# Optimization experiments

Measured on AMD Instinct MI355X. Metric: run time of the kernel, lower is better.

## Reference

```python
import jax, jax.numpy as jnp
import numpy as np
from jax import lax

T, B, D_IN, D_DAY, H, D_OUT = 64, 32, 4096, 256, 256, 942


def setup_inputs() -> dict:
    key = jax.random.key(0)
    ks = jax.random.split(key, 18)
    s = 0.05
    def rn(k, shape):
        return jax.random.normal(k, shape, jnp.float32) * s
    return {
        "x": jax.random.uniform(ks[0], (T, B, D_IN), jnp.float32),
        "W_emb": rn(ks[1], (D_DAY, D_IN)), "b_emb": rn(ks[2], (D_DAY,)),
        "Wih_f": rn(ks[3], (3 * H, D_DAY)), "Whh_f": rn(ks[4], (3 * H, H)),
        "bih_f": rn(ks[5], (3 * H,)), "bhh_f": rn(ks[6], (3 * H,)),
        "Wih_r": rn(ks[7], (3 * H, D_DAY)), "Whh_r": rn(ks[8], (3 * H, H)),
        "bih_r": rn(ks[9], (3 * H,)), "bhh_r": rn(ks[10], (3 * H,)),
        "attn_w": rn(ks[11], (2 * H,)), "attn_b": rn(ks[12], ()),
        "W_ao": rn(ks[13], (D_DAY, 4 * H)), "b_ao": rn(ks[14], (D_DAY,)),
        "W_o": rn(ks[15], (D_OUT, D_DAY)), "b_o": rn(ks[16], (D_OUT,)),
    }


def _gru_cell(xt, h, Wih, Whh, bih, bhh):
    # PyTorch nn.GRU cell math
    gi = xt @ Wih.T + bih          # [B, 3H]
    gh = h @ Whh.T + bhh           # [B, 3H]
    ir, iz, inn = jnp.split(gi, 3, axis=-1)
    hr, hz, hn = jnp.split(gh, 3, axis=-1)
    r = jax.nn.sigmoid(ir + hr)
    z = jax.nn.sigmoid(iz + hz)
    n = jnp.tanh(inn + r * hn)
    return (1.0 - z) * n + z * h


def _run_gru(seq, Wih, Whh, bih, bhh):
    # seq: [L, B, D] -> all hidden states [L, B, H], h0 = zeros
    h0 = jnp.zeros((seq.shape[1], H), seq.dtype)
    def step(h, xt):
        h2 = _gru_cell(xt, h, Wih, Whh, bih, bhh)
        return h2, h2
    return lax.scan(step, h0, seq)[1]


def reference(x, W_emb, b_emb, Wih_f, Whh_f, bih_f, bhh_f,
              Wih_r, Whh_r, bih_r, bhh_r, attn_w, attn_b,
              W_ao, b_ao, W_o, b_o):
    day_emb = jnp.einsum('tbi,di->tbd', x, W_emb) + b_emb       # [T,B,Dday]

    # Forward GRU over the prefix [:i+1] equals the first i+1 states of one full run.
    fwd = _run_gru(day_emb, Wih_f, Whh_f, bih_f, bhh_f)          # [T,B,H]

    # Reverse GRU is recomputed per timestep on the flipped prefix (O(T^2)).
    i_idx = jnp.arange(T)
    j_idx = jnp.arange(T)
    gather = jnp.clip(i_idx[:, None] - j_idx[None, :], 0)        # [T,T]
    rev_in = day_emb[gather]                                     # [T,T,B,Dday]; row i, step j = day_emb[i-j]
    rev = jax.vmap(lambda s: _run_gru(s, Wih_r, Whh_r, bih_r, bhh_r))(rev_in)  # [T,T,B,H]

    # Attention scores on concat(fwd, rev) without materializing the 2H concat:
    w_f, w_r = attn_w[:H], attn_w[H:]
    scores = (jnp.einsum('tbh,h->tb', fwd, w_f)[None, :, :]
              + jnp.einsum('itbh,h->itb', rev, w_r) + attn_b)    # [T(i),T(t),B]
    valid = j_idx[None, :] <= i_idx[:, None]                     # t <= i
    scores = jnp.where(valid[:, :, None], scores, -jnp.inf)
    alpha = jax.nn.softmax(scores, axis=1)                       # softmax over prefix time

    counts = (i_idx + 1).astype(day_emb.dtype)[:, None, None]    # mean over i+1 steps
    c_fwd = jnp.einsum('itb,tbh->ibh', alpha, fwd) / counts      # [T,B,H]
    c_rev = jnp.einsum('itb,itbh->ibh', alpha, rev) / counts     # [T,B,H]
    rev_last = rev[i_idx, i_idx]                                 # rnn_h[-1] reverse half, [T,B,H]

    h_t = jnp.concatenate([c_fwd, c_rev, fwd, rev_last], axis=-1)  # [T,B,4H]
    h_t_out = h_t @ W_ao.T + b_ao                                # [T,B,Dday]
    return jax.nn.sigmoid(h_t_out @ W_o.T + b_o)                 # [T,B,D_OUT]
```

## Files before the change

### kernel.cpp

```cpp
#include <hip/hip_runtime.h>
#include <hip/hip_bf16.h>


typedef __bf16 bf16x8 __attribute__((ext_vector_type(8)));
typedef __bf16 bf16x4 __attribute__((ext_vector_type(4)));
typedef float  f32x4  __attribute__((ext_vector_type(4)));
typedef int    int4v  __attribute__((ext_vector_type(4)));

static constexpr float NEG_L2E = -1.442695041f;
static constexpr float TWO_L2E =  2.885390082f;

static constexpr size_t OFF_PK_EMB = 0;
static constexpr size_t OFF_PK_IH  = 2097152;
static constexpr size_t OFF_WQ     = 2883584;
static constexpr size_t OFF_WSC    = 3276800;
static constexpr size_t OFF_PK_AO  = 3670016;
static constexpr size_t OFF_PK_O   = 4194304;
static constexpr size_t OFF_DAY    = 4685824;
static constexpr size_t OFF_GIT    = 5734400;
static constexpr size_t OFF_BC     = 12025856;
static constexpr size_t OFF_REV    = 18317312;
static constexpr size_t OFF_FWD    = 52396032;
static constexpr size_t OFF_HT     = 53444608;
static constexpr size_t OFF_TMP1   = 57638912;
static constexpr size_t OFF_XB     = OFF_REV;

__device__ __forceinline__ float sigf(float x) {
    return __builtin_amdgcn_rcpf(1.f + __expf(-x));
}

#define LDS_BARRIER() asm volatile("s_waitcnt lgkmcnt(0)\n\ts_barrier" ::: "memory")

__global__ __launch_bounds__(256) void pack_misc(
    const float* __restrict__ We,  const float* __restrict__ Wir, const float* __restrict__ Wif,
    const float* __restrict__ Wao, const float* __restrict__ Wo,  const float* __restrict__ x,
    const float* __restrict__ Whr, const float* __restrict__ Whf,
    const float* __restrict__ bih_r, const float* __restrict__ bih_f,
    const float* __restrict__ bhh_r, const float* __restrict__ bhh_f,
    __bf16* pe, __bf16* pi, __bf16* pao, __bf16* po, __bf16* xb,
    signed char* __restrict__ wq, float* __restrict__ wscale, float* __restrict__ bc)
{
    int b = blockIdx.x;
    if (b >= 5048) {
        int rowb = (b - 5048) * 4 + (threadIdx.x >> 6);
        int t = threadIdx.x & 63;
        int dir = (rowb >= 768) ? 1 : 0;
        int n = rowb - dir * 768;
        const float* src = (dir ? Whf : Whr) + (size_t)n * 256;
        float4 wv = ((const float4*)src)[t];
        float m = fmaxf(fmaxf(fabsf(wv.x), fabsf(wv.y)), fmaxf(fabsf(wv.z), fabsf(wv.w)));
#pragma unroll
        for (int off = 32; off > 0; off >>= 1) m = fmaxf(m, __shfl_xor(m, off));
        m = fmaxf(m, 1e-20f);
        float inv = 127.f / m;
        int q0 = (int)__builtin_rintf(wv.x * inv);
        int q1 = (int)__builtin_rintf(wv.y * inv);
        int q2 = (int)__builtin_rintf(wv.z * inv);
        int q3 = (int)__builtin_rintf(wv.w * inv);
        int pk = (q0 & 0xff) | ((q1 & 0xff) << 8) | ((q2 & 0xff) << 16) | ((q3 & 0xff) << 24);
        int dlane = (n & 15) | (((t >> 2) & 3) << 4);
        size_t byte = (size_t)dir * 196608 + ((size_t)(n >> 4) * 4 + (t >> 4)) * 1024
                    + (size_t)dlane * 16 + (t & 3) * 4;
        *(int*)(wq + byte) = pk;
        if (t == 0) {
            float gc = (n < 512) ? NEG_L2E : TWO_L2E;
            wscale[rowb] = m * (1.f / 16129.f) * gc;
            const float* bi = dir ? bih_f : bih_r;
            const float* bh = dir ? bhh_f : bhh_r;
            bc[rowb] = (n < 512) ? (bi[n] + bh[n]) * NEG_L2E : bi[n] * TWO_L2E;
        }
        return;
    }
    if (b >= 952) {
        size_t base = ((size_t)(b - 952) * 256 + threadIdx.x) * 8;
        float4 v0 = *(const float4*)(x + base);
        float4 v1 = *(const float4*)(x + base + 4);
        bf16x8 o;
        o[0]=(__bf16)v0.x; o[1]=(__bf16)v0.y; o[2]=(__bf16)v0.z; o[3]=(__bf16)v0.w;
        o[4]=(__bf16)v1.x; o[5]=(__bf16)v1.y; o[6]=(__bf16)v1.z; o[7]=(__bf16)v1.w;
        *(bf16x8*)(xb + base) = o;
        return;
    }
    const float* src; __bf16* dst; int Nsrc, k32l, b0; bool ih = false;
    if (b < 512)      { src = We;  dst = pe;          Nsrc = 256; k32l = 7; b0 = 0;   }
    else if (b < 608) { src = Wir; dst = pi;          Nsrc = 768; k32l = 3; b0 = 512; ih = true; }
    else if (b < 704) { src = Wif; dst = pi + 196608; Nsrc = 768; k32l = 3; b0 = 608; ih = true; }
    else if (b < 832) { src = Wao; dst = pao;         Nsrc = 256; k32l = 5; b0 = 704; }
    else              { src = Wo;  dst = po;          Nsrc = 942; k32l = 3; b0 = 832; }
    int t8   = (b - b0) * 256 + threadIdx.x;
    int lane = t8 & 63;
    int K32  = 1 << k32l;
    int K    = K32 << 5;
    int ks   = (t8 >> 6) & (K32 - 1);
    int nt   = t8 >> (6 + k32l);
    int n    = nt * 16 + (lane & 15);
    int k0   = ks * 32 + ((lane >> 4) << 3);
    bf16x8 o;
    if (n < Nsrc) {
        const float* sp = src + (size_t)n * K + k0;
        float4 v0 = *(const float4*)sp;
        float4 v1 = *(const float4*)(sp + 4);
        float s = ih ? ((n < 512) ? NEG_L2E : TWO_L2E) : 1.f;
        o[0]=(__bf16)(v0.x*s); o[1]=(__bf16)(v0.y*s); o[2]=(__bf16)(v0.z*s); o[3]=(__bf16)(v0.w*s);
        o[4]=(__bf16)(v1.x*s); o[5]=(__bf16)(v1.y*s); o[6]=(__bf16)(v1.z*s); o[7]=(__bf16)(v1.w*s);
    } else {
#pragma unroll
        for (int q = 0; q < 8; q++) o[q] = (__bf16)0.f;
    }
    *(bf16x8*)(dst + (size_t)t8 * 8) = o;
}

template<int MODE, int KDIM, int NTILES, int CSTRIDE, int NREAL>
__global__ __launch_bounds__(256) void gemm_k(
    const __bf16* __restrict__ Ap, const __bf16* __restrict__ Bp, void* __restrict__ Cp,
    const float* __restrict__ bias)
{
    __shared__ __align__(16) __bf16 As[32][88];
    const int tid = threadIdx.x;
    const int w = tid >> 6, lane = tid & 63, c = lane & 15, quad = lane >> 4;
    const int mb = blockIdx.x, nb = blockIdx.y;
    constexpr int K32 = KDIM / 32;
    constexpr int NK  = KDIM / 64;
    constexpr int NT_W = NTILES / 2;
    const int wrow = w & 1, ncol0 = (w >> 1) * NT_W;

    f32x4 acc[NT_W];
#pragma unroll
    for (int nt = 0; nt < NT_W; nt++) acc[nt] = (f32x4){0.f, 0.f, 0.f, 0.f};

    const int row = tid >> 3, kp = (tid & 7) * 8;
    uint4 pb;
    auto issue  = [&](int kb) { pb = *(const uint4*)(Ap + (size_t)(mb * 32 + row) * KDIM + kb * 64 + kp); };
    auto commit = [&]() { *(uint4*)&As[row][kp] = pb; };

    bf16x8 bcur[2][NT_W], bnxt[2][NT_W];
    auto loadB = [&](int kb, bf16x8 (&dst)[2][NT_W]) {
#pragma unroll
        for (int kk = 0; kk < 2; kk++)
#pragma unroll
            for (int nt = 0; nt < NT_W; nt++)
                dst[kk][nt] = *(const bf16x8*)(Bp +
                    ((size_t)((nb * NTILES + ncol0 + nt) * K32 + kb * 2 + kk) * 64 + lane) * 8);
    };

    issue(0);
    loadB(0, bcur);
    for (int kb = 0; kb < NK; kb++) {
        commit();
        __syncthreads();
        if (kb + 1 < NK) { issue(kb + 1); loadB(kb + 1, bnxt); }
#pragma unroll
        for (int kk = 0; kk < 2; kk++) {
            bf16x8 a = *(const bf16x8*)&As[wrow * 16 + c][kk * 32 + quad * 8];
#pragma unroll
            for (int nt = 0; nt < NT_W; nt++)
                acc[nt] = __builtin_amdgcn_mfma_f32_16x16x32_bf16(a, bcur[kk][nt], acc[nt], 0, 0, 0);
        }
        if (kb + 1 < NK) {
#pragma unroll
            for (int kk = 0; kk < 2; kk++)
#pragma unroll
                for (int nt = 0; nt < NT_W; nt++) bcur[kk][nt] = bnxt[kk][nt];
        }
        __syncthreads();
    }

#pragma unroll
    for (int nt = 0; nt < NT_W; nt++) {
        int n = nb * (NTILES * 16) + (ncol0 + nt) * 16 + c;
        float bv = (n < NREAL) ? bias[n] : 0.f;
#pragma unroll
        for (int r0 = 0; r0 < 4; r0++) {
            int m = mb * 32 + wrow * 16 + quad * 4 + r0;
            float v = acc[nt][r0] + bv;
            if constexpr (MODE == 0) ((__bf16*)Cp)[(size_t)m * CSTRIDE + n] = (__bf16)v;
            else { if (n < NREAL) ((float*)Cp)[(size_t)m * CSTRIDE + n] = sigf(v); }
        }
    }
}

__global__ __launch_bounds__(1024, 4) void gru_recurrent(
    const signed char* __restrict__ wq, const float* __restrict__ wscale,
    const float* __restrict__ bhh_r, const float* __restrict__ bhh_f,
    const __bf16* __restrict__ Gi,
    __bf16* __restrict__ revb, __bf16* __restrict__ fwdb)
{
    __shared__ __align__(16) signed char hbuf[2][16][272];
    const int tid = threadIdx.x;
    const int w = tid >> 6, lane = tid & 63, c = lane & 15, quad = lane >> 4;
    const int bid = blockIdx.x;
    const bool isF = (bid < 2);
    const int ia = isF ? 63 : (63 - ((bid - 2) >> 1));
    const int b0 = (bid & 1) << 4;
    const int steps = ia + 1;
    const float* bhh = isF ? bhh_f : bhh_r;
    __bf16* outb = isF ? fwdb : (revb + ((size_t)(ia * (ia + 1) / 2)) * 8192);
    const int dirb = isF ? 768 : 0;

    const int4v* pw = (const int4v*)(wq + (isF ? 196608 : 0));
    int4v bw[3][4];
#pragma unroll
    for (int g = 0; g < 3; g++)
#pragma unroll
        for (int ks = 0; ks < 4; ks++)
            bw[g][ks] = pw[(size_t)((g * 16 + w) * 4 + ks) * 64 + lane];

    const int dq = (w << 4) + (quad << 2);
    f32x4 sc[3];
#pragma unroll
    for (int g = 0; g < 3; g++) sc[g] = *(const f32x4*)&wscale[dirb + g * 256 + dq];
    f32x4 bnv = *(const f32x4*)&bhh[512 + dq];
#pragma unroll
    for (int q = 0; q < 4; q++) bnv[q] *= TWO_L2E;

    float hreg[4] = {0.f, 0.f, 0.f, 0.f};
    for (int idx = tid; idx < 2 * 16 * 272 / 4; idx += 1024) ((int*)hbuf)[idx] = 0;
    __syncthreads();

    const __bf16* grow = Gi + (size_t)((isF ? 0 : ia) * 32 + b0 + c) * 1536 + dirb + dq;
    const long gstep = isF ? (32 * 1536) : -(32 * 1536);
    __bf16* go = outb + (size_t)(b0 + c) * 256 + dq;

    bf16x4 gcur[3], gnxt[3];
#pragma unroll
    for (int g = 0; g < 3; g++) gcur[g] = *(const bf16x4*)(grow + g * 256);

    for (int j = 0; j < steps; j++) {
        const int rb = j & 1, wbuf = rb ^ 1;
        const bool more = (j + 1 < steps);

        if (more) {
            grow += gstep;
#pragma unroll
            for (int g = 0; g < 3; g++) gnxt[g] = *(const bf16x4*)(grow + g * 256);
        }

        int4v a0 = {0,0,0,0}, a1 = {0,0,0,0}, a2 = {0,0,0,0};
#pragma unroll
        for (int ks = 0; ks < 4; ks++) {
            int4v av = *(const int4v*)&hbuf[rb][c][ks * 64 + (quad << 4)];
            a0 = __builtin_amdgcn_mfma_i32_16x16x64_i8(bw[0][ks], av, a0, 0, 0, 0);
            a1 = __builtin_amdgcn_mfma_i32_16x16x64_i8(bw[1][ks], av, a1, 0, 0, 0);
            a2 = __builtin_amdgcn_mfma_i32_16x16x64_i8(bw[2][ks], av, a2, 0, 0, 0);
        }

        int pk = 0;
        bf16x4 hb;
#pragma unroll
        for (int r0 = 0; r0 < 4; r0++) {
            float er = __builtin_amdgcn_exp2f(fmaf((float)a0[r0], sc[0][r0], (float)gcur[0][r0]));
            float rg = __builtin_amdgcn_rcpf(1.f + er);
            float ez = __builtin_amdgcn_exp2f(fmaf((float)a1[r0], sc[1][r0], (float)gcur[1][r0]));
            float zg = __builtin_amdgcn_rcpf(1.f + ez);
            float narg = fmaf(rg, fmaf((float)a2[r0], sc[2][r0], bnv[r0]), (float)gcur[2][r0]);
            float en = __builtin_amdgcn_exp2f(narg);
            float ng = fmaf(-2.f, __builtin_amdgcn_rcpf(1.f + en), 1.f);
            float h  = fmaf(zg, hreg[r0] - ng, ng);
            hreg[r0] = h;
            int q = (int)__builtin_rintf(h * 127.f);
            pk |= (q & 0xff) << (8 * r0);
            hb[r0] = (__bf16)h;
        }
        *(int*)&hbuf[wbuf][c][dq] = pk;
        *(bf16x4*)go = hb;
        go += 8192;
        LDS_BARRIER();
        if (more) {
#pragma unroll
            for (int g = 0; g < 3; g++) gcur[g] = gnxt[g];
        }
    }
}

__global__ __launch_bounds__(512) void attn_kernel(
    const __bf16* __restrict__ revb, const __bf16* __restrict__ fwdb,
    const float* __restrict__ attn_w, const float* __restrict__ attn_bp,
    __bf16* __restrict__ ht)
{
    const int tid = threadIdx.x;
    const int w = tid >> 6, lane = tid & 63;
    const int wid = blockIdx.x * 8 + w;
    const int i = wid >> 5, b = wid & 31;
    const int d0 = lane * 4;

    float wf[4], wr[4];
#pragma unroll
    for (int q = 0; q < 4; q++) { wf[q] = attn_w[d0 + q]; wr[q] = attn_w[256 + d0 + q]; }
    const float ab = attn_bp[0];
    const __bf16* rp = revb + ((size_t)(i * (i + 1) / 2)) * 8192 + (size_t)b * 256 + d0;
    const __bf16* fp = fwdb + (size_t)b * 256 + d0;

    float mx = -1e30f, l = 0.f;
    float cf[4] = {0,0,0,0}, cr[4] = {0,0,0,0};
    bf16x4 rn = *(const bf16x4*)rp, fn = *(const bf16x4*)fp;
    for (int t = 0; t <= i; t++) {
        bf16x4 rv4 = rn, fv4 = fn;
        if (t < i) {
            rn = *(const bf16x4*)(rp + (size_t)(t + 1) * 8192);
            fn = *(const bf16x4*)(fp + (size_t)(t + 1) * 8192);
        }
        float rv[4], fv[4], s = 0.f;
#pragma unroll
        for (int q = 0; q < 4; q++) {
            rv[q] = (float)rv4[q]; fv[q] = (float)fv4[q];
            s += rv[q] * wr[q] + fv[q] * wf[q];
        }
#pragma unroll
        for (int off = 32; off > 0; off >>= 1) s += __shfl_xor(s, off);
        s += ab;
        float mn = fmaxf(mx, s);
        float scl = __expf(mx - mn);
        float p  = __expf(s - mn);
        l = l * scl + p;
#pragma unroll
        for (int q = 0; q < 4; q++) { cf[q] = cf[q] * scl + p * fv[q]; cr[q] = cr[q] * scl + p * rv[q]; }
        mx = mn;
    }
    float inv = __builtin_amdgcn_rcpf(l * (float)(i + 1));
    __bf16* hp = ht + (size_t)(i * 32 + b) * 1024 + d0;
    const __bf16* fl = fp + (size_t)i * 8192;
    const __bf16* rl = rp + (size_t)i * 8192;
#pragma unroll
    for (int q = 0; q < 4; q++) {
        hp[q]       = (__bf16)(cf[q] * inv);
        hp[256 + q] = (__bf16)(cr[q] * inv);
        hp[512 + q] = fl[q];
        hp[768 + q] = rl[q];
    }
}

extern "C" void kernel_launch(void* const* d_in, const int* in_sizes, int n_in,
                              void* d_out, int out_size, void* d_ws, size_t ws_size,
                              hipStream_t stream) {
    const float* x      = (const float*)d_in[0];
    const float* W_emb  = (const float*)d_in[1];
    const float* b_emb  = (const float*)d_in[2];
    const float* Wih_f  = (const float*)d_in[3];
    const float* Whh_f  = (const float*)d_in[4];
    const float* bih_f  = (const float*)d_in[5];
    const float* bhh_f  = (const float*)d_in[6];
    const float* Wih_r  = (const float*)d_in[7];
    const float* Whh_r  = (const float*)d_in[8];
    const float* bih_r  = (const float*)d_in[9];
    const float* bhh_r  = (const float*)d_in[10];
    const float* attn_w = (const float*)d_in[11];
    const float* attn_b = (const float*)d_in[12];
    const float* W_ao   = (const float*)d_in[13];
    const float* b_ao   = (const float*)d_in[14];
    const float* W_o    = (const float*)d_in[15];
    const float* b_o    = (const float*)d_in[16];
    float* out = (float*)d_out;

    char* ws = (char*)d_ws;
    __bf16* pk_emb = (__bf16*)(ws + OFF_PK_EMB);
    __bf16* pk_ih  = (__bf16*)(ws + OFF_PK_IH);
    signed char* wq = (signed char*)(ws + OFF_WQ);
    float*  wsc    = (float*)(ws + OFF_WSC);
    __bf16* pk_ao  = (__bf16*)(ws + OFF_PK_AO);
    __bf16* pk_o   = (__bf16*)(ws + OFF_PK_O);
    __bf16* day    = (__bf16*)(ws + OFF_DAY);
    __bf16* Gi     = (__bf16*)(ws + OFF_GIT);
    float*  bc     = (float*)(ws + OFF_BC);
    __bf16* revb   = (__bf16*)(ws + OFF_REV);
    __bf16* fwdb   = (__bf16*)(ws + OFF_FWD);
    __bf16* ht     = (__bf16*)(ws + OFF_HT);
    __bf16* tmp1   = (__bf16*)(ws + OFF_TMP1);
    __bf16* xb     = (__bf16*)(ws + OFF_XB);

    pack_misc<<<5432, 256, 0, stream>>>(W_emb, Wih_r, Wih_f, W_ao, W_o, x,
                                        Whh_r, Whh_f, bih_r, bih_f, bhh_r, bhh_f,
                                        pk_emb, pk_ih, pk_ao, pk_o, xb, wq, wsc, bc);

    gemm_k<0, 4096, 4, 256, 256><<<dim3(64, 4), 256, 0, stream>>>(xb, pk_emb, day, b_emb);
    gemm_k<0, 256, 4, 1536, 1536><<<dim3(64, 24), 256, 0, stream>>>(day, pk_ih, Gi, bc);

    gru_recurrent<<<130, 1024, 0, stream>>>(wq, wsc, bhh_r, bhh_f, Gi, revb, fwdb);

    attn_kernel<<<256, 512, 0, stream>>>(revb, fwdb, attn_w, attn_b, ht);

    gemm_k<0, 1024, 4, 256, 256><<<dim3(64, 4), 256, 0, stream>>>(ht, pk_ao, tmp1, b_ao);
    gemm_k<1, 256, 4, 942, 942><<<dim3(64, 15), 256, 0, stream>>>(tmp1, pk_o, out, b_o);
}
```

Before: 325.4 us.

## Interleave two independent GRU sequences per block to hide recurrent latency

Each recurrent block now runs two independent GRU chains (two reverse prefix lengths, or both forward batch halves) interleaved in one time loop, halving the grid from 130 to 65 blocks. The second chain's MFMA and gate math can fill the latency bubbles of the first, and the per-step barrier is shared between them. The int8 quantisation of h is done with a magic-number add and byte-perm instead of rint/shift/or, and the LDS hidden-state buffer layout changes to a contiguous lane-indexed form. In exchange each block does roughly twice the work per step, uses more registers, and the pairing of uneven sequence lengths leaves some idle steps.

```diff
diff --git a/kernel.cpp b/kernel.cpp
--- a/kernel.cpp
+++ b/kernel.cpp
@@ -179,23 +179,56 @@
     }
 }
 
+__device__ __forceinline__ void gru_cell4(
+    const int4v a0, const int4v a1, const int4v a2,
+    const f32x4 sc0, const f32x4 sc1, const f32x4 sc2, const f32x4 bnv,
+    const bf16x4 g0, const bf16x4 g1, const bf16x4 g2,
+    float* hreg, int* pk, bf16x4* hb)
+{
+    float f[4];
+#pragma unroll
+    for (int r = 0; r < 4; r++) {
+        float er = __builtin_amdgcn_exp2f(fmaf((float)a0[r], sc0[r], (float)g0[r]));
+        float rg = __builtin_amdgcn_rcpf(1.f + er);
+        float ez = __builtin_amdgcn_exp2f(fmaf((float)a1[r], sc1[r], (float)g1[r]));
+        float zg = __builtin_amdgcn_rcpf(1.f + ez);
+        float narg = fmaf(rg, fmaf((float)a2[r], sc2[r], bnv[r]), (float)g2[r]);
+        float en = __builtin_amdgcn_exp2f(narg);
+        float ng = fmaf(-2.f, __builtin_amdgcn_rcpf(1.f + en), 1.f);
+        float h  = fmaf(zg, hreg[r] - ng, ng);
+        hreg[r] = h;
+        (*hb)[r] = (__bf16)h;
+        f[r] = fmaf(h, 127.f, 12582912.f);
+    }
+    unsigned lo = __builtin_amdgcn_perm(__float_as_uint(f[1]), __float_as_uint(f[0]), 0x00000400u);
+    unsigned hi = __builtin_amdgcn_perm(__float_as_uint(f[3]), __float_as_uint(f[2]), 0x04000000u);
+    *pk = (int)__builtin_amdgcn_perm(hi, lo, 0x07060100u);
+}
+
 __global__ __launch_bounds__(1024, 4) void gru_recurrent(
     const signed char* __restrict__ wq, const float* __restrict__ wscale,
     const float* __restrict__ bhh_r, const float* __restrict__ bhh_f,
     const __bf16* __restrict__ Gi,
     __bf16* __restrict__ revb, __bf16* __restrict__ fwdb)
 {
-    __shared__ __align__(16) signed char hbuf[2][16][272];
+    __shared__ __align__(16) signed char hA[2][4096];
+    __shared__ __align__(16) signed char hB[2][4096];
     const int tid = threadIdx.x;
     const int w = tid >> 6, lane = tid & 63, c = lane & 15, quad = lane >> 4;
     const int bid = blockIdx.x;
-    const bool isF = (bid < 2);
-    const int ia = isF ? 63 : (63 - ((bid - 2) >> 1));
-    const int b0 = (bid & 1) << 4;
-    const int steps = ia + 1;
+    const bool isF = (bid == 0);
+    int iaA, iaB, b0A, b0B;
+    if (isF) { iaA = 63; iaB = 63; b0A = 0; b0B = 16; }
+    else {
+        int r = bid - 1, k = r >> 1, half = r & 1;
+        iaA = 63 - 2 * k; iaB = iaA - 1;
+        b0A = half << 4;  b0B = b0A;
+    }
+    const int sA = iaA + 1, sB = iaB + 1;
     const float* bhh = isF ? bhh_f : bhh_r;
-    __bf16* outb = isF ? fwdb : (revb + ((size_t)(ia * (ia + 1) / 2)) * 8192);
     const int dirb = isF ? 768 : 0;
+    __bf16* outA = isF ? fwdb : (revb + (size_t)(iaA * (iaA + 1) / 2) * 8192);
+    __bf16* outB = isF ? fwdb : (revb + (size_t)(iaB * (iaB + 1) / 2) * 8192);
 
     const int4v* pw = (const int4v*)(wq + (isF ? 196608 : 0));
     int4v bw[3][4];
@@ -206,69 +239,79 @@
             bw[g][ks] = pw[(size_t)((g * 16 + w) * 4 + ks) * 64 + lane];
 
     const int dq = (w << 4) + (quad << 2);
-    f32x4 sc[3];
-#pragma unroll
-    for (int g = 0; g < 3; g++) sc[g] = *(const f32x4*)&wscale[dirb + g * 256 + dq];
+    f32x4 sc0 = *(const f32x4*)&wscale[dirb + dq];
+    f32x4 sc1 = *(const f32x4*)&wscale[dirb + 256 + dq];
+    f32x4 sc2 = *(const f32x4*)&wscale[dirb + 512 + dq];
     f32x4 bnv = *(const f32x4*)&bhh[512 + dq];
 #pragma unroll
     for (int q = 0; q < 4; q++) bnv[q] *= TWO_L2E;
 
-    float hreg[4] = {0.f, 0.f, 0.f, 0.f};
-    for (int idx = tid; idx < 2 * 16 * 272 / 4; idx += 1024) ((int*)hbuf)[idx] = 0;
+    float hrA[4] = {0.f, 0.f, 0.f, 0.f}, hrB[4] = {0.f, 0.f, 0.f, 0.f};
+    ((int*)hA)[tid] = 0; ((int*)hA)[tid + 1024] = 0;
+    ((int*)hB)[tid] = 0; ((int*)hB)[tid + 1024] = 0;
     __syncthreads();
 
-    const __bf16* grow = Gi + (size_t)((isF ? 0 : ia) * 32 + b0 + c) * 1536 + dirb + dq;
+    const __bf16* growA = Gi + (size_t)((isF ? 0 : iaA) * 32 + b0A + c) * 1536 + dirb + dq;
+    const __bf16* growB = Gi + (size_t)((isF ? 0 : iaB) * 32 + b0B + c) * 1536 + dirb + dq;
     const long gstep = isF ? (32 * 1536) : -(32 * 1536);
-    __bf16* go = outb + (size_t)(b0 + c) * 256 + dq;
-
-    bf16x4 gcur[3], gnxt[3];
-#pragma unroll
-    for (int g = 0; g < 3; g++) gcur[g] = *(const bf16x4*)(grow + g * 256);
-
-    for (int j = 0; j < steps; j++) {
-        const int rb = j & 1, wbuf = rb ^ 1;
-        const bool more = (j + 1 < steps);
-
-        if (more) {
-            grow += gstep;
-#pragma unroll
-            for (int g = 0; g < 3; g++) gnxt[g] = *(const bf16x4*)(grow + g * 256);
-        }
+    __bf16* goA = outA + (size_t)(b0A + c) * 256 + dq;
+    __bf16* goB = outB + (size_t)(b0B + c) * 256 + dq;
+
+    bf16x4 gA[3], gB[3];
+#pragma unroll
+    for (int g = 0; g < 3; g++) gA[g] = *(const bf16x4*)(growA + g * 256);
+#pragma unroll
+    for (int g = 0; g < 3; g++) gB[g] = *(const bf16x4*)(growB + g * 256);
+
+    const int wr_off = (w >> 2) * 1024 + ((c + ((w & 3) << 4)) << 4) + (quad << 2);
+    const int rd_off = lane << 4;
+
+    for (int j = 0; j < sA; j++) {
+        const int rb = j & 1, wb = rb ^ 1;
+        const bool doB   = (j < sB);
+        const bool moreA = (j + 1 < sA), moreB = (j + 1 < sB);
 
         int4v a0 = {0,0,0,0}, a1 = {0,0,0,0}, a2 = {0,0,0,0};
 #pragma unroll
         for (int ks = 0; ks < 4; ks++) {
-            int4v av = *(const int4v*)&hbuf[rb][c][ks * 64 + (quad << 4)];
+            int4v av = *(const int4v*)&hA[rb][ks * 1024 + rd_off];
             a0 = __builtin_amdgcn_mfma_i32_16x16x64_i8(bw[0][ks], av, a0, 0, 0, 0);
             a1 = __builtin_amdgcn_mfma_i32_16x16x64_i8(bw[1][ks], av, a1, 0, 0, 0);
             a2 = __builtin_amdgcn_mfma_i32_16x16x64_i8(bw[2][ks], av, a2, 0, 0, 0);
         }
-
-        int pk = 0;
-        bf16x4 hb;
-#pragma unroll
-        for (int r0 = 0; r0 < 4; r0++) {
-            float er = __builtin_amdgcn_exp2f(fmaf((float)a0[r0], sc[0][r0], (float)gcur[0][r0]));
-            float rg = __builtin_amdgcn_rcpf(1.f + er);
-            float ez = __builtin_amdgcn_exp2f(fmaf((float)a1[r0], sc[1][r0], (float)gcur[1][r0]));
-            float zg = __builtin_amdgcn_rcpf(1.f + ez);
-            float narg = fmaf(rg, fmaf((float)a2[r0], sc[2][r0], bnv[r0]), (float)gcur[2][r0]);
-            float en = __builtin_amdgcn_exp2f(narg);
-            float ng = fmaf(-2.f, __builtin_amdgcn_rcpf(1.f + en), 1.f);
-            float h  = fmaf(zg, hreg[r0] - ng, ng);
-            hreg[r0] = h;
-            int q = (int)__builtin_rintf(h * 127.f);
-            pk |= (q & 0xff) << (8 * r0);
-            hb[r0] = (__bf16)h;
-        }
-        *(int*)&hbuf[wbuf][c][dq] = pk;
-        *(bf16x4*)go = hb;
-        go += 8192;
+        int pkA; bf16x4 hbA;
+        gru_cell4(a0, a1, a2, sc0, sc1, sc2, bnv, gA[0], gA[1], gA[2], hrA, &pkA, &hbA);
+        *(int*)&hA[wb][wr_off] = pkA;
+
+        int pkB; bf16x4 hbB;
+        if (doB) {
+            int4v b0 = {0,0,0,0}, b1 = {0,0,0,0}, b2 = {0,0,0,0};
+#pragma unroll
+            for (int ks = 0; ks < 4; ks++) {
+                int4v av = *(const int4v*)&hB[rb][ks * 1024 + rd_off];
+                b0 = __builtin_amdgcn_mfma_i32_16x16x64_i8(bw[0][ks], av, b0, 0, 0, 0);
+                b1 = __builtin_amdgcn_mfma_i32_16x16x64_i8(bw[1][ks], av, b1, 0, 0, 0);
+                b2 = __builtin_amdgcn_mfma_i32_16x16x64_i8(bw[2][ks], av, b2, 0, 0, 0);
+            }
+            gru_cell4(b0, b1, b2, sc0, sc1, sc2, bnv, gB[0], gB[1], gB[2], hrB, &pkB, &hbB);
+            *(int*)&hB[wb][wr_off] = pkB;
+        }
+
+        if (moreA) {
+            growA += gstep;
+#pragma unroll
+            for (int g = 0; g < 3; g++) gA[g] = *(const bf16x4*)(growA + g * 256);
+        }
+        if (moreB) {
+            growB += gstep;
+#pragma unroll
+            for (int g = 0; g < 3; g++) gB[g] = *(const bf16x4*)(growB + g * 256);
+        }
+
+        *(bf16x4*)goA = hbA; goA += 8192;
+        if (doB) { *(bf16x4*)goB = hbB; goB += 8192; }
+
         LDS_BARRIER();
-        if (more) {
-#pragma unroll
-            for (int g = 0; g < 3; g++) gcur[g] = gnxt[g];
-        }
     }
 }
 
@@ -374,7 +417,7 @@
     gemm_k<0, 4096, 4, 256, 256><<<dim3(64, 4), 256, 0, stream>>>(xb, pk_emb, day, b_emb);
     gemm_k<0, 256, 4, 1536, 1536><<<dim3(64, 24), 256, 0, stream>>>(day, pk_ih, Gi, bc);
 
-    gru_recurrent<<<130, 1024, 0, stream>>>(wq, wsc, bhh_r, bhh_f, Gi, revb, fwdb);
+    gru_recurrent<<<65, 1024, 0, stream>>>(wq, wsc, bhh_r, bhh_f, Gi, revb, fwdb);
 
     attn_kernel<<<256, 512, 0, stream>>>(revb, fwdb, attn_w, attn_b, ht);
 
```

Result: slower. 418.1 us (+28.5%).
